# Kernel tuning notes

Measured on AMD Instinct MI355X. Metric: run time of the kernel, lower is better.

The kernel has to match this reference:

```python
import jax, jax.numpy as jnp
import numpy as np

N_NODES = 50000
N_EDGES = 800000
IN, HID, OUT = 128, [128, 128], 64


def setup_inputs() -> dict:
    key = jax.random.key(0)
    ks = jax.random.split(key, 10)
    inp = {
        'in_feat': jax.random.normal(ks[0], (N_NODES, IN), dtype=jnp.float32),
        'src': jax.random.randint(ks[1], (N_EDGES,), 0, N_NODES, dtype=jnp.int32),
        'dst': jax.random.randint(ks[2], (N_EDGES,), 0, N_NODES, dtype=jnp.int32),
    }
    dims = [IN] + HID + [OUT]  # [128,128,128,64]
    for i in range(3):
        fan_in = dims[i]
        inp[f'W{i}'] = jax.random.normal(ks[3 + i], (dims[i + 1], dims[i]), dtype=jnp.float32) / np.sqrt(fan_in)
        inp[f'b{i}'] = jnp.zeros((dims[i + 1],), dtype=jnp.float32)
    return inp


def _sage_gcn_layer(x, W, b, src, dst, n_nodes):
    # DGL SAGEConv aggregator_type='gcn':
    #   neigh = segment_sum of src feats over dst edges (graph already has self-loops)
    #   h = (neigh + x) / (in_degree + 1); out = h @ W.T + b
    msg = x[src]                                             # [E, d] gather
    neigh = jax.ops.segment_sum(msg, dst, num_segments=n_nodes)
    deg = jax.ops.segment_sum(jnp.ones(src.shape[0], x.dtype), dst, num_segments=n_nodes)
    h = (neigh + x) / (deg[:, None] + 1.0)
    return h @ W.T + b


def reference(in_feat, src, dst, W0, b0, W1, b1, W2, b2):
    n = in_feat.shape[0]
    # remove_self_loop + add_self_loop -> exactly one self loop per node
    loop = jnp.arange(n, dtype=src.dtype)
    src_f = jnp.concatenate([src, loop])
    dst_f = jnp.concatenate([dst, loop])
    # Dropout(0.5) is identity in eval mode.
    h = in_feat
    h = jax.nn.relu(_sage_gcn_layer(h, W0, b0, src_f, dst_f, n))
    h = jax.nn.relu(_sage_gcn_layer(h, W1, b1, src_f, dst_f, n))
    h = _sage_gcn_layer(h, W2, b2, src_f, dst_f, n)
    return h
```

## Files before the change

kernel.cpp:

```cpp
#include <hip/hip_runtime.h>
#include <hip/hip_bf16.h>


#define NFEAT 128
#define BKT_CAP 12288
#define CHUNK 64

using bf16x8 = __attribute__((ext_vector_type(8))) short;
using f32x4  = __attribute__((ext_vector_type(4))) float;

__device__ __forceinline__ ushort f2bf(float f) {
    unsigned u = __float_as_uint(f);
    u = (u + 0x7fffu + ((u >> 16) & 1u)) >> 16;
    return (ushort)u;
}
__device__ __forceinline__ float bflo(unsigned v) { return __uint_as_float(v << 16); }
__device__ __forceinline__ float bfhi(unsigned v) { return __uint_as_float(v & 0xffff0000u); }

__device__ __forceinline__ int xcc_id() {
    int x;
    asm volatile("s_getreg_b32 %0, hwreg(HW_REG_XCC_ID)" : "=s"(x));
    return x & 7;
}


__global__ __launch_bounds__(256) void k_init(unsigned* __restrict__ esrc_u32, int fillN, unsigned sent2,
                                              int* __restrict__ ctl, ushort* __restrict__ Ybuf, int n,
                                              const float* __restrict__ W0, const float* __restrict__ W1,
                                              const float* __restrict__ W2, ushort* __restrict__ Wb) {
    int i = blockIdx.x * 256 + threadIdx.x;
    if (i < fillN) {
        esrc_u32[i] = sent2;
    } else if (i < fillN + 336) {
        ctl[i - fillN] = 0;
    } else if (i < fillN + 336 + 64) {
        int j = i - fillN - 336;
        int p = j >> 4, k = j & 15;
        ((unsigned*)(Ybuf + (size_t)p * (n + 1) * 32 + (size_t)n * 32))[k] = 0u;
    } else if (i < fillN + 336 + 64 + 40960) {
        int j = i - fillN - 336 - 64;
        float v = (j < 16384) ? W0[j] : ((j < 32768) ? W1[j - 16384] : W2[j - 32768]);
        Wb[j] = f2bf(v);
    }
}


__global__ __launch_bounds__(256) void k_bin(const int* __restrict__ src, const int* __restrict__ dst,
                                             int* __restrict__ gcur, unsigned* __restrict__ pairs, int ne) {
    __shared__ int lcnt[128];
    __shared__ int lbase[128];
    int tid = threadIdx.x;
    if (tid < 128) lcnt[tid] = 0;
    __syncthreads();
    int e0 = blockIdx.x * 4096;
    int myrank[16];
    int mybkt[16];
    unsigned mypair[16];
    #pragma unroll
    for (int i = 0; i < 16; ++i) {
        int e = e0 + tid + i * 256;
        if (e < ne) {
            int s = src[e], d = dst[e];
            int b = d >> 9;
            mybkt[i]  = b;
            mypair[i] = (unsigned)(s & 0xffff) | ((unsigned)(d & 511) << 16);
            myrank[i] = atomicAdd(&lcnt[b], 1);
        } else mybkt[i] = -1;
    }
    __syncthreads();
    if (tid < 128) lbase[tid] = lcnt[tid] ? atomicAdd(&gcur[tid], lcnt[tid]) : 0;
    __syncthreads();
    #pragma unroll
    for (int i = 0; i < 16; ++i) {
        if (mybkt[i] >= 0) {
            int pos = lbase[mybkt[i]] + myrank[i];
            if (pos < BKT_CAP) pairs[(size_t)mybkt[i] * BKT_CAP + pos] = mypair[i];
        }
    }
}


__global__ __launch_bounds__(1024) void k_cntprep(const unsigned* __restrict__ pairs, const int* __restrict__ gcur,
                                                  int* __restrict__ cnt, int* __restrict__ perm,
                                                  int* __restrict__ offs, int* __restrict__ gbase, int n) {
    __shared__ int lcnt[1024];
    __shared__ int hist[256];
    __shared__ int hcur[256];
    __shared__ int wtot[16];
    __shared__ int wpre[16];
    __shared__ int sbase;
    int tid  = threadIdx.x;
    int lane = tid & 63;
    int wv   = tid >> 6;
    int base = blockIdx.x * 1024;
    lcnt[tid] = 0;
    if (tid < 256) hist[tid] = 0;
    __syncthreads();
    #pragma unroll
    for (int h = 0; h < 2; ++h) {
        int bkt = blockIdx.x * 2 + h;
        int m = gcur[bkt];
        if (m > BKT_CAP) m = BKT_CAP;
        const unsigned* p = pairs + (size_t)bkt * BKT_CAP;
        for (int i = tid; i < m; i += 1024)
            atomicAdd(&lcnt[(int)(p[i] >> 16) + h * 512], 1);
    }
    __syncthreads();
    int i   = base + tid;
    bool act = i < n;
    int c = act ? lcnt[tid] : 0;
    if (act) cnt[i] = c;
    int d = c > 255 ? 255 : c;
    int rank = 0;
    if (act) rank = atomicAdd(&hist[d], 1);
    __syncthreads();
    {
        int v = (tid < 256) ? hist[tid] : 0;
        int val = v;
        #pragma unroll
        for (int off = 1; off < 64; off <<= 1) {
            int t = __shfl_up(val, off);
            if (lane >= off) val += t;
        }
        if (lane == 63) wtot[wv] = val;
        __syncthreads();
        if (tid == 0) {
            int s = 0;
            #pragma unroll
            for (int w = 0; w < 4; ++w) { wpre[w] = s; s += wtot[w]; }
        }
        __syncthreads();
        if (tid < 256) hcur[tid] = val - v + wpre[wv];
        __syncthreads();
        if (act) perm[base + hcur[d] + rank] = i;
        __syncthreads();
    }
    {
        int p8 = act ? ((c + 7) & ~7) : 0;
        int val = p8;
        #pragma unroll
        for (int off = 1; off < 64; off <<= 1) {
            int t = __shfl_up(val, off);
            if (lane >= off) val += t;
        }
        if (lane == 63) wtot[wv] = val;
        __syncthreads();
        if (tid == 0) {
            int s = 0;
            #pragma unroll
            for (int w = 0; w < 16; ++w) { wpre[w] = s; s += wtot[w]; }
            sbase = atomicAdd(gbase, s);
        }
        __syncthreads();
        if (act) offs[i] = sbase + val - p8 + wpre[wv];
    }
}


__global__ __launch_bounds__(256) void k_scatter(const unsigned* __restrict__ pairs, const int* __restrict__ gcur,
                                                 const int* __restrict__ offs, ushort* __restrict__ esrc, int n) {
    __shared__ int lcur[512];
    __shared__ int loffs[512];
    int b = blockIdx.x, tid = threadIdx.x;
    int base = b * 512;
    for (int i = tid; i < 512; i += 256) {
        lcur[i] = 0;
        int node = base + i;
        loffs[i] = (node < n) ? offs[node] : 0;
    }
    __syncthreads();
    int m = gcur[b];
    if (m > BKT_CAP) m = BKT_CAP;
    const unsigned* p = pairs + (size_t)b * BKT_CAP;
    for (int i = tid; i < m; i += 256) {
        unsigned pr = p[i];
        int dlow = pr >> 16;
        int r = atomicAdd(&lcur[dlow], 1);
        esrc[loffs[dlow] + r] = (ushort)(pr & 0xffffu);
    }
}


template <typename InT, int N, bool PLANES_IN>
__global__ __launch_bounds__(256) void k_gemm_mfma(const InT* __restrict__ X, const ushort* __restrict__ Wb,
                                                   ushort* __restrict__ Y, int M, int Mp) {
    int w    = threadIdx.x >> 6;
    int lane = threadIdx.x & 63;
    int kb   = (lane >> 4) * 8;
    int rbase = blockIdx.x * 128 + w * 16 + (lane & 15);

    bf16x8 a0[4], a1[4];
    #pragma unroll
    for (int set = 0; set < 2; ++set) {
        int rowf = rbase + set * 64;
        bf16x8* a = set ? a1 : a0;
        if (rowf < M) {
            #pragma unroll
            for (int ks = 0; ks < 4; ++ks) {
                if constexpr (PLANES_IN) {
                    a[ks] = *(const bf16x8*)((const ushort*)X + (size_t)ks * Mp * 32 + (size_t)rowf * 32 + kb);
                } else {
                    const float* xp = (const float*)X + (size_t)rowf * 128 + ks * 32 + kb;
                    float4 f0 = *(const float4*)xp;
                    float4 f1 = *(const float4*)(xp + 4);
                    bf16x8 t;
                    t[0] = f2bf(f0.x); t[1] = f2bf(f0.y); t[2] = f2bf(f0.z); t[3] = f2bf(f0.w);
                    t[4] = f2bf(f1.x); t[5] = f2bf(f1.y); t[6] = f2bf(f1.z); t[7] = f2bf(f1.w);
                    a[ks] = t;
                }
            }
        } else {
            #pragma unroll
            for (int ks = 0; ks < 4; ++ks) {
                bf16x8 z = {0, 0, 0, 0, 0, 0, 0, 0};
                a[ks] = z;
            }
        }
    }

    constexpr int NT = N / 16;
    f32x4 acc0[NT], acc1[NT];
    #pragma unroll
    for (int nt = 0; nt < NT; ++nt) {
        acc0[nt] = (f32x4){0.f, 0.f, 0.f, 0.f};
        acc1[nt] = (f32x4){0.f, 0.f, 0.f, 0.f};
    }

    #pragma unroll
    for (int nt = 0; nt < NT; ++nt) {
        const ushort* wp = Wb + (size_t)(nt * 16 + (lane & 15)) * 128 + kb;
        #pragma unroll
        for (int ks = 0; ks < 4; ++ks) {
            bf16x8 b = *(const bf16x8*)(wp + ks * 32);
            acc0[nt] = __builtin_amdgcn_mfma_f32_16x16x32_bf16(a0[ks], b, acc0[nt], 0, 0, 0);
            acc1[nt] = __builtin_amdgcn_mfma_f32_16x16x32_bf16(a1[ks], b, acc1[nt], 0, 0, 0);
        }
    }

    int c  = lane & 15;
    int rr = blockIdx.x * 128 + w * 16 + (lane >> 4) * 4;
    #pragma unroll
    for (int set = 0; set < 2; ++set) {
        f32x4* acc = set ? acc1 : acc0;
        #pragma unroll
        for (int j = 0; j < 4; ++j) {
            int r = rr + set * 64 + j;
            if (r < M) {
                #pragma unroll
                for (int nt = 0; nt < NT; ++nt)
                    Y[(size_t)(nt >> 1) * Mp * 32 + (size_t)r * 32 + (nt & 1) * 16 + c] = (ushort)f2bf(acc[nt][j]);
            }
        }
    }
}


#define ACC8(T)  { a0 += bflo((T).x); a1 += bfhi((T).x); a2 += bflo((T).y); a3 += bfhi((T).y); \
                   a4 += bflo((T).z); a5 += bfhi((T).z); a6 += bflo((T).w); a7 += bfhi((T).w); }

template <bool RELU>
__global__ __launch_bounds__(256) void k_agg128(const ushort* __restrict__ Yp, const int* __restrict__ offs,
                                                const int* __restrict__ cnt, const ushort* __restrict__ esrc,
                                                const float* __restrict__ bias, ushort* __restrict__ Zp,
                                                const int* __restrict__ perm, int* __restrict__ qh,
                                                int n, int nchunk) {
    __shared__ int sQ, sT;
    if (threadIdx.x == 0) {
        int pref = xcc_id() & 3;
        int t = -1, qsel = 0;
        #pragma unroll
        for (int a = 0; a < 4; ++a) {
            int cand = (pref + a) & 3;
            int tt = atomicAdd(&qh[cand * 16], 1);
            if (tt < nchunk) { qsel = cand; t = tt; break; }
        }
        sQ = qsel; sT = t;
    }
    __syncthreads();
    int q = sQ, t = sT;
    if (t < 0) return;
    int lane = threadIdx.x & 63;
    int wv   = threadIdx.x >> 6;
    int g    = lane >> 2;
    int sub  = lane & 3;
    int idx  = t * CHUNK + wv * 16 + g;
    bool active = idx < n;
    int nd = 0, start = 0, deg = 0;
    if (active) {
        nd    = perm[idx];
        start = offs[nd];
        deg   = cnt[nd];
    }
    const uint4* Y4 = (const uint4*)(Yp + (size_t)q * (n + 1) * 32);
    uint4*       Z4 = (uint4*)(Zp + (size_t)q * (n + 1) * 32);

    float a0 = 0.f, a1 = 0.f, a2 = 0.f, a3 = 0.f, a4 = 0.f, a5 = 0.f, a6 = 0.f, a7 = 0.f;

    int nblk = active ? ((deg + 7) >> 3) : 0;
    const uint4* ep = (const uint4*)(esrc + start);
    uint4 ib = ep[0];
    #pragma unroll 2
    for (int b = 0; b < nblk; ++b) {
        uint4 ibn = ep[b + 1];
        unsigned s0 = ib.x & 0xffffu, s1 = ib.x >> 16;
        unsigned s2 = ib.y & 0xffffu, s3 = ib.y >> 16;
        unsigned s4 = ib.z & 0xffffu, s5 = ib.z >> 16;
        unsigned s6 = ib.w & 0xffffu, s7 = ib.w >> 16;
        uint4 t0 = Y4[(size_t)s0 * 4 + sub];
        uint4 t1 = Y4[(size_t)s1 * 4 + sub];
        uint4 t2 = Y4[(size_t)s2 * 4 + sub];
        uint4 t3 = Y4[(size_t)s3 * 4 + sub];
        uint4 t4 = Y4[(size_t)s4 * 4 + sub];
        uint4 t5 = Y4[(size_t)s5 * 4 + sub];
        uint4 t6 = Y4[(size_t)s6 * 4 + sub];
        uint4 t7 = Y4[(size_t)s7 * 4 + sub];
        ACC8(t0); ACC8(t1); ACC8(t2); ACC8(t3); ACC8(t4); ACC8(t5); ACC8(t6); ACC8(t7);
        ib = ibn;
    }

    if (active) {
        float scale = 1.0f / (float)(deg + 2);
        uint4 sf = Y4[(size_t)nd * 4 + sub];
        int f0 = q * 32 + sub * 8;
        float4 bA = *(const float4*)&bias[f0];
        float4 bB = *(const float4*)&bias[f0 + 4];
        float r0 = (a0 + 2.f * bflo(sf.x)) * scale + bA.x;
        float r1 = (a1 + 2.f * bfhi(sf.x)) * scale + bA.y;
        float r2 = (a2 + 2.f * bflo(sf.y)) * scale + bA.z;
        float r3 = (a3 + 2.f * bfhi(sf.y)) * scale + bA.w;
        float r4 = (a4 + 2.f * bflo(sf.z)) * scale + bB.x;
        float r5 = (a5 + 2.f * bfhi(sf.z)) * scale + bB.y;
        float r6 = (a6 + 2.f * bflo(sf.w)) * scale + bB.z;
        float r7 = (a7 + 2.f * bfhi(sf.w)) * scale + bB.w;
        if (RELU) {
            r0 = fmaxf(r0, 0.f); r1 = fmaxf(r1, 0.f); r2 = fmaxf(r2, 0.f); r3 = fmaxf(r3, 0.f);
            r4 = fmaxf(r4, 0.f); r5 = fmaxf(r5, 0.f); r6 = fmaxf(r6, 0.f); r7 = fmaxf(r7, 0.f);
        }
        uint4 o;
        o.x = (unsigned)f2bf(r0) | ((unsigned)f2bf(r1) << 16);
        o.y = (unsigned)f2bf(r2) | ((unsigned)f2bf(r3) << 16);
        o.z = (unsigned)f2bf(r4) | ((unsigned)f2bf(r5) << 16);
        o.w = (unsigned)f2bf(r6) | ((unsigned)f2bf(r7) << 16);
        Z4[(size_t)nd * 4 + sub] = o;
    }
}

__global__ __launch_bounds__(256) void k_agg64(const ushort* __restrict__ Yp, const int* __restrict__ offs,
                                               const int* __restrict__ cnt, const ushort* __restrict__ esrc,
                                               const float* __restrict__ bias, float* __restrict__ Z,
                                               const int* __restrict__ perm, int* __restrict__ qh,
                                               int n, int nchunk) {
    __shared__ int sQ, sT;
    if (threadIdx.x == 0) {
        int pref = xcc_id() & 1;
        int t = -1, qsel = 0;
        #pragma unroll
        for (int a = 0; a < 2; ++a) {
            int cand = (pref + a) & 1;
            int tt = atomicAdd(&qh[cand * 16], 1);
            if (tt < nchunk) { qsel = cand; t = tt; break; }
        }
        sQ = qsel; sT = t;
    }
    __syncthreads();
    int h = sQ, t = sT;
    if (t < 0) return;
    int lane = threadIdx.x & 63;
    int wv   = threadIdx.x >> 6;
    int g    = lane >> 2;
    int sub  = lane & 3;
    int idx  = t * CHUNK + wv * 16 + g;
    bool active = idx < n;
    int nd = 0, start = 0, deg = 0;
    if (active) {
        nd    = perm[idx];
        start = offs[nd];
        deg   = cnt[nd];
    }
    const uint4* Y4 = (const uint4*)(Yp + (size_t)h * (n + 1) * 32);

    float a0 = 0.f, a1 = 0.f, a2 = 0.f, a3 = 0.f, a4 = 0.f, a5 = 0.f, a6 = 0.f, a7 = 0.f;

    int nblk = active ? ((deg + 7) >> 3) : 0;
    const uint4* ep = (const uint4*)(esrc + start);
    uint4 ib = ep[0];
    #pragma unroll 2
    for (int b = 0; b < nblk; ++b) {
        uint4 ibn = ep[b + 1];
        unsigned s0 = ib.x & 0xffffu, s1 = ib.x >> 16;
        unsigned s2 = ib.y & 0xffffu, s3 = ib.y >> 16;
        unsigned s4 = ib.z & 0xffffu, s5 = ib.z >> 16;
        unsigned s6 = ib.w & 0xffffu, s7 = ib.w >> 16;
        uint4 t0 = Y4[(size_t)s0 * 4 + sub];
        uint4 t1 = Y4[(size_t)s1 * 4 + sub];
        uint4 t2 = Y4[(size_t)s2 * 4 + sub];
        uint4 t3 = Y4[(size_t)s3 * 4 + sub];
        uint4 t4 = Y4[(size_t)s4 * 4 + sub];
        uint4 t5 = Y4[(size_t)s5 * 4 + sub];
        uint4 t6 = Y4[(size_t)s6 * 4 + sub];
        uint4 t7 = Y4[(size_t)s7 * 4 + sub];
        ACC8(t0); ACC8(t1); ACC8(t2); ACC8(t3); ACC8(t4); ACC8(t5); ACC8(t6); ACC8(t7);
        ib = ibn;
    }

    if (active) {
        float scale = 1.0f / (float)(deg + 2);
        uint4 sf = Y4[(size_t)nd * 4 + sub];
        int f0 = h * 32 + sub * 8;
        float4 bA = *(const float4*)&bias[f0];
        float4 bB = *(const float4*)&bias[f0 + 4];
        float4 oA, oB;
        oA.x = (a0 + 2.f * bflo(sf.x)) * scale + bA.x;
        oA.y = (a1 + 2.f * bfhi(sf.x)) * scale + bA.y;
        oA.z = (a2 + 2.f * bflo(sf.y)) * scale + bA.z;
        oA.w = (a3 + 2.f * bfhi(sf.y)) * scale + bA.w;
        oB.x = (a4 + 2.f * bflo(sf.z)) * scale + bB.x;
        oB.y = (a5 + 2.f * bfhi(sf.z)) * scale + bB.y;
        oB.z = (a6 + 2.f * bflo(sf.w)) * scale + bB.z;
        oB.w = (a7 + 2.f * bfhi(sf.w)) * scale + bB.w;
        float* zr = Z + (size_t)nd * 64 + f0;
        *(float4*)zr       = oA;
        *(float4*)(zr + 4) = oB;
    }
}


extern "C" void kernel_launch(void* const* d_in, const int* in_sizes, int n_in,
                              void* d_out, int out_size, void* d_ws, size_t ws_size,
                              hipStream_t stream) {
    const float* in_feat = (const float*)d_in[0];
    const int*   src     = (const int*)d_in[1];
    const int*   dst     = (const int*)d_in[2];
    const float* W0      = (const float*)d_in[3];
    const float* b0      = (const float*)d_in[4];
    const float* W1      = (const float*)d_in[5];
    const float* b1      = (const float*)d_in[6];
    const float* W2      = (const float*)d_in[7];
    const float* b2      = (const float*)d_in[8];
    float* out = (float*)d_out;

    const int n  = in_sizes[0] / NFEAT;
    const int ne = in_sizes[1];
    const int nch = (n + 1023) / 1024;
    const int NB  = (n + 511) >> 9;
    const int nchunk = (n + CHUNK - 1) / CHUNK;
    const int escap = (ne + 8 * n + 31) & ~15;

    int* offs       = (int*)d_ws;
    int* gcur       = offs + ((n + 4) & ~3);
    int* qh         = gcur + 128;
    int* gbase      = qh + 192;
    int* cnt        = gbase + 16;
    int* perm       = cnt + ((n + 3) & ~3);
    unsigned* pairs = (unsigned*)(perm + ((n + 3) & ~3));
    ushort* esrc    = (ushort*)(pairs + (size_t)128 * BKT_CAP);
    ushort* Wb      = esrc + escap;
    ushort* Ybuf    = Wb + 40960;
    ushort* Zbuf    = Ybuf + (size_t)(n + 1) * NFEAT;

    const int fillN = escap / 2;
    const unsigned sent2 = ((unsigned)n << 16) | (unsigned)n;
    const int initN = fillN + 336 + 64 + 40960;
    k_init<<<(initN + 255) / 256, 256, 0, stream>>>((unsigned*)esrc, fillN, sent2, gcur, Ybuf, n,
                                                    W0, W1, W2, Wb);

    k_bin<<<(ne + 4095) / 4096, 256, 0, stream>>>(src, dst, gcur, pairs, ne);
    k_cntprep<<<nch, 1024, 0, stream>>>(pairs, gcur, cnt, perm, offs, gbase, n);
    k_scatter<<<NB, 256, 0, stream>>>(pairs, gcur, offs, esrc, n);

    const ushort* Wb0 = Wb;
    const ushort* Wb1 = Wb + 16384;
    const ushort* Wb2 = Wb + 32768;

    const int gg = (n + 127) / 128;
    const int Mp = n + 1;

    k_gemm_mfma<float, 128, false><<<gg, 256, 0, stream>>>(in_feat, Wb0, Ybuf, n, Mp);
    k_agg128<true><<<4 * nchunk, 256, 0, stream>>>(Ybuf, offs, cnt, esrc, b0, Zbuf, perm, qh, n, nchunk);
    k_gemm_mfma<ushort, 128, true><<<gg, 256, 0, stream>>>(Zbuf, Wb1, Ybuf, n, Mp);
    k_agg128<true><<<4 * nchunk, 256, 0, stream>>>(Ybuf, offs, cnt, esrc, b1, Zbuf, perm, qh + 64, n, nchunk);
    k_gemm_mfma<ushort, 64, true><<<gg, 256, 0, stream>>>(Zbuf, Wb2, Ybuf, n, Mp);
    k_agg64<<<2 * nchunk, 256, 0, stream>>>(Ybuf, offs, cnt, esrc, b2, out, perm, qh + 128, n, nchunk);

    (void)ws_size; (void)n_in; (void)out_size;
}
```

Before: 200.0 us.

## Fuse scatter into cntprep, persistent agg kernels, vectorize binning, stream GEMM stores

Merges the edge scatter into the count/prefix kernel so bucket pairs are written to the CSR array in the same launch, using shared-memory offsets. The aggregation kernels become persistent: a fixed grid of blocks loops, pulling chunks from atomic work queues instead of one block per chunk. Edge binning now loads src/dst with int4 vector loads, and the GEMM stores each output tile right after its MFMAs, which cuts live accumulator registers. The costs are an extra launch boundary removed versus heavier per-block work, and queue contention in the persistent loop.

```diff
diff --git a/kernel.cpp b/kernel.cpp
--- a/kernel.cpp
+++ b/kernel.cpp
@@ -57,15 +57,31 @@
     int mybkt[16];
     unsigned mypair[16];
     #pragma unroll
-    for (int i = 0; i < 16; ++i) {
-        int e = e0 + tid + i * 256;
-        if (e < ne) {
-            int s = src[e], d = dst[e];
-            int b = d >> 9;
-            mybkt[i]  = b;
-            mypair[i] = (unsigned)(s & 0xffff) | ((unsigned)(d & 511) << 16);
-            myrank[i] = atomicAdd(&lcnt[b], 1);
-        } else mybkt[i] = -1;
+    for (int blk = 0; blk < 4; ++blk) {
+        int e = e0 + blk * 1024 + tid * 4;
+        int4 s4, d4;
+        bool full = (e + 3 < ne);
+        if (full) {
+            s4 = *(const int4*)&src[e];
+            d4 = *(const int4*)&dst[e];
+        } else {
+            s4.x = (e + 0 < ne) ? src[e + 0] : 0;  d4.x = (e + 0 < ne) ? dst[e + 0] : -1;
+            s4.y = (e + 1 < ne) ? src[e + 1] : 0;  d4.y = (e + 1 < ne) ? dst[e + 1] : -1;
+            s4.z = (e + 2 < ne) ? src[e + 2] : 0;  d4.z = (e + 2 < ne) ? dst[e + 2] : -1;
+            s4.w = (e + 3 < ne) ? src[e + 3] : 0;  d4.w = (e + 3 < ne) ? dst[e + 3] : -1;
+        }
+        int ss[4] = {s4.x, s4.y, s4.z, s4.w};
+        int dd[4] = {d4.x, d4.y, d4.z, d4.w};
+        #pragma unroll
+        for (int c = 0; c < 4; ++c) {
+            int i = blk * 4 + c;
+            if (dd[c] >= 0) {
+                int b = dd[c] >> 9;
+                mybkt[i]  = b;
+                mypair[i] = (unsigned)(ss[c] & 0xffff) | ((unsigned)(dd[c] & 511) << 16);
+                myrank[i] = atomicAdd(&lcnt[b], 1);
+            } else mybkt[i] = -1;
+        }
     }
     __syncthreads();
     if (tid < 128) lbase[tid] = lcnt[tid] ? atomicAdd(&gcur[tid], lcnt[tid]) : 0;
@@ -82,8 +98,10 @@
 
 __global__ __launch_bounds__(1024) void k_cntprep(const unsigned* __restrict__ pairs, const int* __restrict__ gcur,
                                                   int* __restrict__ cnt, int* __restrict__ perm,
-                                                  int* __restrict__ offs, int* __restrict__ gbase, int n) {
+                                                  int* __restrict__ offs, int* __restrict__ gbase,
+                                                  ushort* __restrict__ esrc, int n) {
     __shared__ int lcnt[1024];
+    __shared__ int loffs[1024];
     __shared__ int hist[256];
     __shared__ int hcur[256];
     __shared__ int wtot[16];
@@ -152,31 +170,24 @@
             sbase = atomicAdd(gbase, s);
         }
         __syncthreads();
-        if (act) offs[i] = sbase + val - p8 + wpre[wv];
-    }
-}
-
-
-__global__ __launch_bounds__(256) void k_scatter(const unsigned* __restrict__ pairs, const int* __restrict__ gcur,
-                                                 const int* __restrict__ offs, ushort* __restrict__ esrc, int n) {
-    __shared__ int lcur[512];
-    __shared__ int loffs[512];
-    int b = blockIdx.x, tid = threadIdx.x;
-    int base = b * 512;
-    for (int i = tid; i < 512; i += 256) {
-        lcur[i] = 0;
-        int node = base + i;
-        loffs[i] = (node < n) ? offs[node] : 0;
-    }
-    __syncthreads();
-    int m = gcur[b];
-    if (m > BKT_CAP) m = BKT_CAP;
-    const unsigned* p = pairs + (size_t)b * BKT_CAP;
-    for (int i = tid; i < m; i += 256) {
-        unsigned pr = p[i];
-        int dlow = pr >> 16;
-        int r = atomicAdd(&lcur[dlow], 1);
-        esrc[loffs[dlow] + r] = (ushort)(pr & 0xffffu);
+        int myoff = sbase + val - p8 + wpre[wv];
+        if (act) offs[i] = myoff;
+        loffs[tid] = myoff;
+        lcnt[tid]  = 0;
+    }
+    __syncthreads();
+    #pragma unroll
+    for (int h = 0; h < 2; ++h) {
+        int bkt = blockIdx.x * 2 + h;
+        int m = gcur[bkt];
+        if (m > BKT_CAP) m = BKT_CAP;
+        const unsigned* p = pairs + (size_t)bkt * BKT_CAP;
+        for (int j = tid; j < m; j += 1024) {
+            unsigned pr = p[j];
+            int w = (int)(pr >> 16) + h * 512;
+            int r = atomicAdd(&lcnt[w], 1);
+            esrc[loffs[w] + r] = (ushort)(pr & 0xffffu);
+        }
     }
 }
 
@@ -219,37 +230,29 @@
     }
 
     constexpr int NT = N / 16;
-    f32x4 acc0[NT], acc1[NT];
+    int c  = lane & 15;
+    int rr = blockIdx.x * 128 + w * 16 + (lane >> 4) * 4;
     #pragma unroll
     for (int nt = 0; nt < NT; ++nt) {
-        acc0[nt] = (f32x4){0.f, 0.f, 0.f, 0.f};
-        acc1[nt] = (f32x4){0.f, 0.f, 0.f, 0.f};
-    }
-
-    #pragma unroll
-    for (int nt = 0; nt < NT; ++nt) {
+        f32x4 acc0 = (f32x4){0.f, 0.f, 0.f, 0.f};
+        f32x4 acc1 = (f32x4){0.f, 0.f, 0.f, 0.f};
         const ushort* wp = Wb + (size_t)(nt * 16 + (lane & 15)) * 128 + kb;
         #pragma unroll
         for (int ks = 0; ks < 4; ++ks) {
             bf16x8 b = *(const bf16x8*)(wp + ks * 32);
-            acc0[nt] = __builtin_amdgcn_mfma_f32_16x16x32_bf16(a0[ks], b, acc0[nt], 0, 0, 0);
-            acc1[nt] = __builtin_amdgcn_mfma_f32_16x16x32_bf16(a1[ks], b, acc1[nt], 0, 0, 0);
-        }
-    }
-
-    int c  = lane & 15;
-    int rr = blockIdx.x * 128 + w * 16 + (lane >> 4) * 4;
-    #pragma unroll
-    for (int set = 0; set < 2; ++set) {
-        f32x4* acc = set ? acc1 : acc0;
+            acc0 = __builtin_amdgcn_mfma_f32_16x16x32_bf16(a0[ks], b, acc0, 0, 0, 0);
+            acc1 = __builtin_amdgcn_mfma_f32_16x16x32_bf16(a1[ks], b, acc1, 0, 0, 0);
+        }
+        size_t pl = (size_t)(nt >> 1) * Mp * 32 + (nt & 1) * 16 + c;
         #pragma unroll
         for (int j = 0; j < 4; ++j) {
-            int r = rr + set * 64 + j;
-            if (r < M) {
-                #pragma unroll
-                for (int nt = 0; nt < NT; ++nt)
-                    Y[(size_t)(nt >> 1) * Mp * 32 + (size_t)r * 32 + (nt & 1) * 16 + c] = (ushort)f2bf(acc[nt][j]);
-            }
+            int r = rr + j;
+            if (r < M)      Y[pl + (size_t)r * 32]        = (ushort)f2bf(acc0[j]);
+        }
+        #pragma unroll
+        for (int j = 0; j < 4; ++j) {
+            int r = rr + 64 + j;
+            if (r < M)      Y[pl + (size_t)r * 32]        = (ushort)f2bf(acc1[j]);
         }
     }
 }
@@ -265,83 +268,89 @@
                                                 const int* __restrict__ perm, int* __restrict__ qh,
                                                 int n, int nchunk) {
     __shared__ int sQ, sT;
-    if (threadIdx.x == 0) {
-        int pref = xcc_id() & 3;
-        int t = -1, qsel = 0;
-        #pragma unroll
-        for (int a = 0; a < 4; ++a) {
-            int cand = (pref + a) & 3;
-            int tt = atomicAdd(&qh[cand * 16], 1);
-            if (tt < nchunk) { qsel = cand; t = tt; break; }
-        }
-        sQ = qsel; sT = t;
-    }
-    __syncthreads();
-    int q = sQ, t = sT;
-    if (t < 0) return;
     int lane = threadIdx.x & 63;
     int wv   = threadIdx.x >> 6;
     int g    = lane >> 2;
     int sub  = lane & 3;
-    int idx  = t * CHUNK + wv * 16 + g;
-    bool active = idx < n;
-    int nd = 0, start = 0, deg = 0;
-    if (active) {
-        nd    = perm[idx];
-        start = offs[nd];
-        deg   = cnt[nd];
-    }
-    const uint4* Y4 = (const uint4*)(Yp + (size_t)q * (n + 1) * 32);
-    uint4*       Z4 = (uint4*)(Zp + (size_t)q * (n + 1) * 32);
-
-    float a0 = 0.f, a1 = 0.f, a2 = 0.f, a3 = 0.f, a4 = 0.f, a5 = 0.f, a6 = 0.f, a7 = 0.f;
-
-    int nblk = active ? ((deg + 7) >> 3) : 0;
-    const uint4* ep = (const uint4*)(esrc + start);
-    uint4 ib = ep[0];
-    #pragma unroll 2
-    for (int b = 0; b < nblk; ++b) {
-        uint4 ibn = ep[b + 1];
-        unsigned s0 = ib.x & 0xffffu, s1 = ib.x >> 16;
-        unsigned s2 = ib.y & 0xffffu, s3 = ib.y >> 16;
-        unsigned s4 = ib.z & 0xffffu, s5 = ib.z >> 16;
-        unsigned s6 = ib.w & 0xffffu, s7 = ib.w >> 16;
-        uint4 t0 = Y4[(size_t)s0 * 4 + sub];
-        uint4 t1 = Y4[(size_t)s1 * 4 + sub];
-        uint4 t2 = Y4[(size_t)s2 * 4 + sub];
-        uint4 t3 = Y4[(size_t)s3 * 4 + sub];
-        uint4 t4 = Y4[(size_t)s4 * 4 + sub];
-        uint4 t5 = Y4[(size_t)s5 * 4 + sub];
-        uint4 t6 = Y4[(size_t)s6 * 4 + sub];
-        uint4 t7 = Y4[(size_t)s7 * 4 + sub];
-        ACC8(t0); ACC8(t1); ACC8(t2); ACC8(t3); ACC8(t4); ACC8(t5); ACC8(t6); ACC8(t7);
-        ib = ibn;
-    }
-
-    if (active) {
-        float scale = 1.0f / (float)(deg + 2);
-        uint4 sf = Y4[(size_t)nd * 4 + sub];
-        int f0 = q * 32 + sub * 8;
-        float4 bA = *(const float4*)&bias[f0];
-        float4 bB = *(const float4*)&bias[f0 + 4];
-        float r0 = (a0 + 2.f * bflo(sf.x)) * scale + bA.x;
-        float r1 = (a1 + 2.f * bfhi(sf.x)) * scale + bA.y;
-        float r2 = (a2 + 2.f * bflo(sf.y)) * scale + bA.z;
-        float r3 = (a3 + 2.f * bfhi(sf.y)) * scale + bA.w;
-        float r4 = (a4 + 2.f * bflo(sf.z)) * scale + bB.x;
-        float r5 = (a5 + 2.f * bfhi(sf.z)) * scale + bB.y;
-        float r6 = (a6 + 2.f * bflo(sf.w)) * scale + bB.z;
-        float r7 = (a7 + 2.f * bfhi(sf.w)) * scale + bB.w;
-        if (RELU) {
-            r0 = fmaxf(r0, 0.f); r1 = fmaxf(r1, 0.f); r2 = fmaxf(r2, 0.f); r3 = fmaxf(r3, 0.f);
-            r4 = fmaxf(r4, 0.f); r5 = fmaxf(r5, 0.f); r6 = fmaxf(r6, 0.f); r7 = fmaxf(r7, 0.f);
-        }
-        uint4 o;
-        o.x = (unsigned)f2bf(r0) | ((unsigned)f2bf(r1) << 16);
-        o.y = (unsigned)f2bf(r2) | ((unsigned)f2bf(r3) << 16);
-        o.z = (unsigned)f2bf(r4) | ((unsigned)f2bf(r5) << 16);
-        o.w = (unsigned)f2bf(r6) | ((unsigned)f2bf(r7) << 16);
-        Z4[(size_t)nd * 4 + sub] = o;
+    int pref = 0;
+    if (threadIdx.x == 0) pref = xcc_id() & 3;
+
+    while (true) {
+        if (threadIdx.x == 0) {
+            int t = -1, qsel = 0;
+            #pragma unroll
+            for (int a = 0; a < 4; ++a) {
+                int cand = (pref + a) & 3;
+                int tt = atomicAdd(&qh[cand * 16], 1);
+                if (tt < nchunk) { qsel = cand; t = tt; break; }
+            }
+            sQ = qsel; sT = t;
+        }
+        __syncthreads();
+        int q = sQ, t = sT;
+        __syncthreads();
+        if (t < 0) return;
+
+        int idx  = t * CHUNK + wv * 16 + g;
+        bool active = idx < n;
+        int nd = 0, start = 0, deg = 0;
+        if (active) {
+            nd    = perm[idx];
+            start = offs[nd];
+            deg   = cnt[nd];
+        }
+        const uint4* Y4 = (const uint4*)(Yp + (size_t)q * (n + 1) * 32);
+        uint4*       Z4 = (uint4*)(Zp + (size_t)q * (n + 1) * 32);
+
+        float a0 = 0.f, a1 = 0.f, a2 = 0.f, a3 = 0.f, a4 = 0.f, a5 = 0.f, a6 = 0.f, a7 = 0.f;
+        int nblk = active ? ((deg + 7) >> 3) : 0;
+        const uint4* ep = (const uint4*)(esrc + start);
+        uint4 ib = ep[0];
+        #pragma unroll 2
+        for (int b = 0; b < nblk; ++b) {
+            uint4 ibn = ep[b + 1];
+            unsigned s0 = ib.x & 0xffffu, s1 = ib.x >> 16;
+            unsigned s2 = ib.y & 0xffffu, s3 = ib.y >> 16;
+            unsigned s4 = ib.z & 0xffffu, s5 = ib.z >> 16;
+            unsigned s6 = ib.w & 0xffffu, s7 = ib.w >> 16;
+            uint4 t0 = Y4[(size_t)s0 * 4 + sub];
+            uint4 t1 = Y4[(size_t)s1 * 4 + sub];
+            uint4 t2 = Y4[(size_t)s2 * 4 + sub];
+            uint4 t3 = Y4[(size_t)s3 * 4 + sub];
+            uint4 t4 = Y4[(size_t)s4 * 4 + sub];
+            uint4 t5 = Y4[(size_t)s5 * 4 + sub];
+            uint4 t6 = Y4[(size_t)s6 * 4 + sub];
+            uint4 t7 = Y4[(size_t)s7 * 4 + sub];
+            ACC8(t0); ACC8(t1); ACC8(t2); ACC8(t3); ACC8(t4); ACC8(t5); ACC8(t6); ACC8(t7);
+            ib = ibn;
+        }
+
+        if (active) {
+            float scale = 1.0f / (float)(deg + 2);
+            uint4 sf = Y4[(size_t)nd * 4 + sub];
+            int f0 = q * 32 + sub * 8;
+            float4 bA = *(const float4*)&bias[f0];
+            float4 bB = *(const float4*)&bias[f0 + 4];
+            float r0 = (a0 + 2.f * bflo(sf.x)) * scale + bA.x;
+            float r1 = (a1 + 2.f * bfhi(sf.x)) * scale + bA.y;
+            float r2 = (a2 + 2.f * bflo(sf.y)) * scale + bA.z;
+            float r3 = (a3 + 2.f * bfhi(sf.y)) * scale + bA.w;
+            float r4 = (a4 + 2.f * bflo(sf.z)) * scale + bB.x;
+            float r5 = (a5 + 2.f * bfhi(sf.z)) * scale + bB.y;
+            float r6 = (a6 + 2.f * bflo(sf.w)) * scale + bB.z;
+            float r7 = (a7 + 2.f * bfhi(sf.w)) * scale + bB.w;
+            if (RELU) {
+                r0 = fmaxf(r0, 0.f); r1 = fmaxf(r1, 0.f); r2 = fmaxf(r2, 0.f); r3 = fmaxf(r3, 0.f);
+                r4 = fmaxf(r4, 0.f); r5 = fmaxf(r5, 0.f); r6 = fmaxf(r6, 0.f); r7 = fmaxf(r7, 0.f);
+            }
+            uint4 o;
+            o.x = (unsigned)f2bf(r0) | ((unsigned)f2bf(r1) << 16);
+            o.y = (unsigned)f2bf(r2) | ((unsigned)f2bf(r3) << 16);
+            o.z = (unsigned)f2bf(r4) | ((unsigned)f2bf(r5) << 16);
+            o.w = (unsigned)f2bf(r6) | ((unsigned)f2bf(r7) << 16);
+            Z4[(size_t)nd * 4 + sub] = o;
+        }
+        __syncthreads();
     }
 }
 
@@ -351,76 +360,82 @@
                                                const int* __restrict__ perm, int* __restrict__ qh,
                                                int n, int nchunk) {
     __shared__ int sQ, sT;
-    if (threadIdx.x == 0) {
-        int pref = xcc_id() & 1;
-        int t = -1, qsel = 0;
-        #pragma unroll
-        for (int a = 0; a < 2; ++a) {
-            int cand = (pref + a) & 1;
-            int tt = atomicAdd(&qh[cand * 16], 1);
-            if (tt < nchunk) { qsel = cand; t = tt; break; }
-        }
-        sQ = qsel; sT = t;
-    }
-    __syncthreads();
-    int h = sQ, t = sT;
-    if (t < 0) return;
     int lane = threadIdx.x & 63;
     int wv   = threadIdx.x >> 6;
     int g    = lane >> 2;
     int sub  = lane & 3;
-    int idx  = t * CHUNK + wv * 16 + g;
-    bool active = idx < n;
-    int nd = 0, start = 0, deg = 0;
-    if (active) {
-        nd    = perm[idx];
-        start = offs[nd];
-        deg   = cnt[nd];
-    }
-    const uint4* Y4 = (const uint4*)(Yp + (size_t)h * (n + 1) * 32);
-
-    float a0 = 0.f, a1 = 0.f, a2 = 0.f, a3 = 0.f, a4 = 0.f, a5 = 0.f, a6 = 0.f, a7 = 0.f;
-
-    int nblk = active ? ((deg + 7) >> 3) : 0;
-    const uint4* ep = (const uint4*)(esrc + start);
-    uint4 ib = ep[0];
-    #pragma unroll 2
-    for (int b = 0; b < nblk; ++b) {
-        uint4 ibn = ep[b + 1];
-        unsigned s0 = ib.x & 0xffffu, s1 = ib.x >> 16;
-        unsigned s2 = ib.y & 0xffffu, s3 = ib.y >> 16;
-        unsigned s4 = ib.z & 0xffffu, s5 = ib.z >> 16;
-        unsigned s6 = ib.w & 0xffffu, s7 = ib.w >> 16;
-        uint4 t0 = Y4[(size_t)s0 * 4 + sub];
-        uint4 t1 = Y4[(size_t)s1 * 4 + sub];
-        uint4 t2 = Y4[(size_t)s2 * 4 + sub];
-        uint4 t3 = Y4[(size_t)s3 * 4 + sub];
-        uint4 t4 = Y4[(size_t)s4 * 4 + sub];
-        uint4 t5 = Y4[(size_t)s5 * 4 + sub];
-        uint4 t6 = Y4[(size_t)s6 * 4 + sub];
-        uint4 t7 = Y4[(size_t)s7 * 4 + sub];
-        ACC8(t0); ACC8(t1); ACC8(t2); ACC8(t3); ACC8(t4); ACC8(t5); ACC8(t6); ACC8(t7);
-        ib = ibn;
-    }
-
-    if (active) {
-        float scale = 1.0f / (float)(deg + 2);
-        uint4 sf = Y4[(size_t)nd * 4 + sub];
-        int f0 = h * 32 + sub * 8;
-        float4 bA = *(const float4*)&bias[f0];
-        float4 bB = *(const float4*)&bias[f0 + 4];
-        float4 oA, oB;
-        oA.x = (a0 + 2.f * bflo(sf.x)) * scale + bA.x;
-        oA.y = (a1 + 2.f * bfhi(sf.x)) * scale + bA.y;
-        oA.z = (a2 + 2.f * bflo(sf.y)) * scale + bA.z;
-        oA.w = (a3 + 2.f * bfhi(sf.y)) * scale + bA.w;
-        oB.x = (a4 + 2.f * bflo(sf.z)) * scale + bB.x;
-        oB.y = (a5 + 2.f * bfhi(sf.z)) * scale + bB.y;
-        oB.z = (a6 + 2.f * bflo(sf.w)) * scale + bB.z;
-        oB.w = (a7 + 2.f * bfhi(sf.w)) * scale + bB.w;
-        float* zr = Z + (size_t)nd * 64 + f0;
-        *(float4*)zr       = oA;
-        *(float4*)(zr + 4) = oB;
+    int pref = 0;
+    if (threadIdx.x == 0) pref = xcc_id() & 1;
+
+    while (true) {
+        if (threadIdx.x == 0) {
+            int t = -1, qsel = 0;
+            #pragma unroll
+            for (int a = 0; a < 2; ++a) {
+                int cand = (pref + a) & 1;
+                int tt = atomicAdd(&qh[cand * 16], 1);
+                if (tt < nchunk) { qsel = cand; t = tt; break; }
+            }
+            sQ = qsel; sT = t;
+        }
+        __syncthreads();
+        int h = sQ, t = sT;
+        __syncthreads();
+        if (t < 0) return;
+
+        int idx  = t * CHUNK + wv * 16 + g;
+        bool active = idx < n;
+        int nd = 0, start = 0, deg = 0;
+        if (active) {
+            nd    = perm[idx];
+            start = offs[nd];
+            deg   = cnt[nd];
+        }
+        const uint4* Y4 = (const uint4*)(Yp + (size_t)h * (n + 1) * 32);
+
+        float a0 = 0.f, a1 = 0.f, a2 = 0.f, a3 = 0.f, a4 = 0.f, a5 = 0.f, a6 = 0.f, a7 = 0.f;
+        int nblk = active ? ((deg + 7) >> 3) : 0;
+        const uint4* ep = (const uint4*)(esrc + start);
+        uint4 ib = ep[0];
+        #pragma unroll 2
+        for (int b = 0; b < nblk; ++b) {
+            uint4 ibn = ep[b + 1];
+            unsigned s0 = ib.x & 0xffffu, s1 = ib.x >> 16;
+            unsigned s2 = ib.y & 0xffffu, s3 = ib.y >> 16;
+            unsigned s4 = ib.z & 0xffffu, s5 = ib.z >> 16;
+            unsigned s6 = ib.w & 0xffffu, s7 = ib.w >> 16;
+            uint4 t0 = Y4[(size_t)s0 * 4 + sub];
+            uint4 t1 = Y4[(size_t)s1 * 4 + sub];
+            uint4 t2 = Y4[(size_t)s2 * 4 + sub];
+            uint4 t3 = Y4[(size_t)s3 * 4 + sub];
+            uint4 t4 = Y4[(size_t)s4 * 4 + sub];
+            uint4 t5 = Y4[(size_t)s5 * 4 + sub];
+            uint4 t6 = Y4[(size_t)s6 * 4 + sub];
+            uint4 t7 = Y4[(size_t)s7 * 4 + sub];
+            ACC8(t0); ACC8(t1); ACC8(t2); ACC8(t3); ACC8(t4); ACC8(t5); ACC8(t6); ACC8(t7);
+            ib = ibn;
+        }
+
+        if (active) {
+            float scale = 1.0f / (float)(deg + 2);
+            uint4 sf = Y4[(size_t)nd * 4 + sub];
+            int f0 = h * 32 + sub * 8;
+            float4 bA = *(const float4*)&bias[f0];
+            float4 bB = *(const float4*)&bias[f0 + 4];
+            float4 oA, oB;
+            oA.x = (a0 + 2.f * bflo(sf.x)) * scale + bA.x;
+            oA.y = (a1 + 2.f * bfhi(sf.x)) * scale + bA.y;
+            oA.z = (a2 + 2.f * bflo(sf.y)) * scale + bA.z;
+            oA.w = (a3 + 2.f * bfhi(sf.y)) * scale + bA.w;
+            oB.x = (a4 + 2.f * bflo(sf.z)) * scale + bB.x;
+            oB.y = (a5 + 2.f * bfhi(sf.z)) * scale + bB.y;
+            oB.z = (a6 + 2.f * bflo(sf.w)) * scale + bB.z;
+            oB.w = (a7 + 2.f * bfhi(sf.w)) * scale + bB.w;
+            float* zr = Z + (size_t)nd * 64 + f0;
+            *(float4*)zr       = oA;
+            *(float4*)(zr + 4) = oB;
+        }
+        __syncthreads();
     }
 }
 
@@ -442,7 +457,6 @@
     const int n  = in_sizes[0] / NFEAT;
     const int ne = in_sizes[1];
     const int nch = (n + 1023) / 1024;
-    const int NB  = (n + 511) >> 9;
     const int nchunk = (n + CHUNK - 1) / CHUNK;
     const int escap = (ne + 8 * n + 31) & ~15;
 
@@ -465,8 +479,7 @@
                                                     W0, W1, W2, Wb);
 
     k_bin<<<(ne + 4095) / 4096, 256, 0, stream>>>(src, dst, gcur, pairs, ne);
-    k_cntprep<<<nch, 1024, 0, stream>>>(pairs, gcur, cnt, perm, offs, gbase, n);
-    k_scatter<<<NB, 256, 0, stream>>>(pairs, gcur, offs, esrc, n);
+    k_cntprep<<<nch, 1024, 0, stream>>>(pairs, gcur, cnt, perm, offs, gbase, esrc, n);
 
     const ushort* Wb0 = Wb;
     const ushort* Wb1 = Wb + 16384;
@@ -476,11 +489,11 @@
     const int Mp = n + 1;
 
     k_gemm_mfma<float, 128, false><<<gg, 256, 0, stream>>>(in_feat, Wb0, Ybuf, n, Mp);
-    k_agg128<true><<<4 * nchunk, 256, 0, stream>>>(Ybuf, offs, cnt, esrc, b0, Zbuf, perm, qh, n, nchunk);
+    k_agg128<true><<<2048, 256, 0, stream>>>(Ybuf, offs, cnt, esrc, b0, Zbuf, perm, qh, n, nchunk);
     k_gemm_mfma<ushort, 128, true><<<gg, 256, 0, stream>>>(Zbuf, Wb1, Ybuf, n, Mp);
-    k_agg128<true><<<4 * nchunk, 256, 0, stream>>>(Ybuf, offs, cnt, esrc, b1, Zbuf, perm, qh + 64, n, nchunk);
+    k_agg128<true><<<2048, 256, 0, stream>>>(Ybuf, offs, cnt, esrc, b1, Zbuf, perm, qh + 64, n, nchunk);
     k_gemm_mfma<ushort, 64, true><<<gg, 256, 0, stream>>>(Zbuf, Wb2, Ybuf, n, Mp);
-    k_agg64<<<2 * nchunk, 256, 0, stream>>>(Ybuf, offs, cnt, esrc, b2, out, perm, qh + 128, n, nchunk);
+    k_agg64<<<1024, 256, 0, stream>>>(Ybuf, offs, cnt, esrc, b2, out, perm, qh + 128, n, nchunk);
 
     (void)ws_size; (void)n_in; (void)out_size;
 }
```

New measurement: 239.4 us. 1.2x slower.
